# Kernel tuning notes

Hardware: AMD Instinct MI355X
Metric: run time of the kernel (lower is better)

Reference implementation:

```python
import jax, jax.numpy as jnp
import numpy as np

CH = 128
C2 = CH // 2
TEMP = 5.0
RATE = 2  # down conv: k=2,s=2,p=0 ; up: convtranspose k=2,s=2,p=0


def _down(x, w, b):
    # Conv2d(ch, ch, kernel=2, stride=2, pad=0) as a patch contraction
    B, C, H, W = x.shape
    xr = x.reshape(B, C, H // 2, 2, W // 2, 2)
    return jnp.einsum('bcipjq,ocpq->boij', xr, w) + b[None, :, None, None]


def _conv1x1(x, w):
    # w: [out, in]
    return jnp.einsum('bchw,oc->bohw', x, w)


def _maxpool2(x):
    B, C, H, W = x.shape
    return x.reshape(B, C, H // 2, 2, W // 2, 2).max(axis=(3, 5))


def _up(x, w, b):
    # ConvTranspose2d(ch, ch, kernel=2, stride=2, pad=0): each pixel -> 2x2 block
    # w: [in, out, 2, 2] (PyTorch layout)
    B, C, H, W = x.shape
    y = jnp.einsum('bchw,copq->bohpwq', x, w).reshape(B, w.shape[1], H * 2, W * 2)
    return y + b[None, :, None, None]


def setup_inputs() -> dict:
    key = jax.random.key(0)
    ks = jax.random.split(key, 12)
    B, H, W = 4, 192, 192
    sc = 0.05
    return {
        'input_x': jax.random.normal(ks[0], (B, CH, H, W), jnp.float32),
        'input_y': jax.random.normal(ks[1], (B, CH, H, W), jnp.float32),
        'down0_w': jax.random.normal(ks[2], (CH, CH, 2, 2), jnp.float32) * sc,
        'down0_b': jax.random.normal(ks[3], (CH,), jnp.float32) * sc,
        'down1_w': jax.random.normal(ks[4], (CH, CH, 2, 2), jnp.float32) * sc,
        'down1_b': jax.random.normal(ks[5], (CH,), jnp.float32) * sc,
        'theta_w': jax.random.normal(ks[6], (C2, CH), jnp.float32) * sc,
        'phi_w': jax.random.normal(ks[7], (C2, CH), jnp.float32) * sc,
        'g_w': jax.random.normal(ks[8], (C2, CH), jnp.float32) * sc,
        'o_w': jax.random.normal(ks[9], (CH, C2), jnp.float32) * sc,
        'up_w': jax.random.normal(ks[10], (CH, CH, 2, 2), jnp.float32) * sc,
        'up_b': jax.random.normal(ks[11], (CH,), jnp.float32) * sc,
        'gamma': jnp.float32(0.5),
    }


def reference(input_x, input_y, down0_w, down0_b, down1_w, down1_b,
              theta_w, phi_w, g_w, o_w, up_w, up_b, gamma):
    x = _down(input_x, down0_w, down0_b)          # [B, CH, h, w]
    y = _down(input_y, down1_w, down1_b)
    B, _, h, w = x.shape
    N = h * w
    M = N // 4

    theta = _conv1x1(x, theta_w).reshape(B, C2, N)          # queries
    phi = _maxpool2(_conv1x1(x, phi_w)).reshape(B, C2, M)   # keys (pooled)
    g = _maxpool2(_conv1x1(y, g_w)).reshape(B, C2, M)       # values (pooled)

    scores = jnp.einsum('bcn,bcm->bnm', theta, phi)          # [B, N, M]
    beta = jax.nn.softmax(TEMP * scores, axis=-1)

    o_map = jnp.einsum('bcm,bnm->bcn', g, beta).reshape(B, C2, h, w)
    o = _conv1x1(o_map, o_w)                                 # [B, CH, h, w]
    out = _up(o, up_w, up_b) + gamma * input_y
    return out
```

## Files before the change

kernel.cpp:

```cpp
#include <hip/hip_runtime.h>
#include <hip/hip_bf16.h>

#define NN    9216
#define MM    2304
#define HW    36864
#define SLABF 4718592
#define TEMPF 5.0f

#define OFF_X   0
#define OFF_Y   4718592
#define OFF_TH  9437184
#define OFF_TP  11796480
#define OFF_PH  14155776
#define OFF_G   14745600
#define OFF_OM  15335424

typedef unsigned short u16;
typedef unsigned int   u32;
typedef __attribute__((ext_vector_type(8))) short bf16x8;
typedef __attribute__((ext_vector_type(4))) float f32x4;

__device__ __forceinline__ u16 f2bf(float f){
  u32 u; __builtin_memcpy(&u,&f,4);
  u32 lsb = (u>>16)&1u; u += 0x7fffu + lsb;
  return (u16)(u>>16);
}
__device__ __forceinline__ u32 pkbf(float a, float b){
  union { __hip_bfloat162 h; u32 u; } v;
  v.h = __float22bfloat162_rn(make_float2(a,b));
  return v.u;
}

__global__ __launch_bounds__(256) void k_down(const float* __restrict__ in,
    const float* __restrict__ w, const float* __restrict__ bias, float* __restrict__ out)
{
  __shared__ __align__(16) float xs[2][6144];
  int blk = blockIdx.x;
  int jt = blk & 1;
  int r1 = blk >> 1;
  int i  = r1 % 96; int b = r1 / 96;
  int t  = threadIdx.x;

  const float* src = in + (size_t)b*128*HW + (size_t)(2*i)*192 + jt*96;

  int cl[3], qq[3];
  #pragma unroll
  for (int k = 0; k < 3; k++) {
    int idx = t + k*256;
    cl[k] = idx / 24;
    qq[k] = idx - cl[k]*24;
  }

  float4 va[3], vb[3];
  #pragma unroll
  for (int k = 0; k < 3; k++) {
    const float* p = src + (size_t)cl[k]*HW + qq[k]*4;
    va[k] = *(const float4*)p;
    vb[k] = *(const float4*)(p + 192);
  }
  #pragma unroll
  for (int k = 0; k < 3; k++) {
    float* d = &xs[0][cl[k]*192 + qq[k]*8];
    *(float4*)d       = make_float4(va[k].x, vb[k].x, va[k].y, vb[k].y);
    *(float4*)(d + 4) = make_float4(va[k].z, vb[k].z, va[k].w, vb[k].w);
  }

  int og = t >> 4, jg = t & 15;
  int o0 = og * 8;
  float acc[8][3];
  #pragma unroll
  for (int oo = 0; oo < 8; oo++)
    #pragma unroll
    for (int jj = 0; jj < 3; jj++) acc[oo][jj] = 0.f;

  const float* wbase = w + (size_t)o0*512;

  for (int ch = 0; ch < 4; ch++) {
    if (ch < 3) {
      #pragma unroll
      for (int k = 0; k < 3; k++) {
        const float* p = src + (size_t)((ch+1)*32 + cl[k])*HW + qq[k]*4;
        va[k] = *(const float4*)p;
        vb[k] = *(const float4*)(p + 192);
      }
    }
    __syncthreads();

    const float* xb = xs[ch & 1];
    const float* wc = wbase + (ch*32)*4;
    for (int c = 0; c < 32; c++) {
      const float* xp = xb + c*192 + jg*12;
      float4 xv0 = *(const float4*)(xp);
      float4 xv1 = *(const float4*)(xp + 4);
      float4 xv2 = *(const float4*)(xp + 8);
      const float* wp = wc + c*4;
      #pragma unroll
      for (int oo = 0; oo < 8; oo++) {
        float4 wv = *(const float4*)(wp + oo*512);
        acc[oo][0] += xv0.x*wv.x + xv0.z*wv.y + xv0.y*wv.z + xv0.w*wv.w;
        acc[oo][1] += xv1.x*wv.x + xv1.z*wv.y + xv1.y*wv.z + xv1.w*wv.w;
        acc[oo][2] += xv2.x*wv.x + xv2.z*wv.y + xv2.y*wv.z + xv2.w*wv.w;
      }
    }

    if (ch < 3) {
      #pragma unroll
      for (int k = 0; k < 3; k++) {
        float* d = &xs[(ch+1) & 1][cl[k]*192 + qq[k]*8];
        *(float4*)d       = make_float4(va[k].x, vb[k].x, va[k].y, vb[k].y);
        *(float4*)(d + 4) = make_float4(va[k].z, vb[k].z, va[k].w, vb[k].w);
      }
    }
  }

  #pragma unroll
  for (int oo = 0; oo < 8; oo++) {
    int o = o0 + oo;
    float bv = bias[o];
    float* op = out + ((size_t)(b*128 + o))*NN + i*96 + jt*48 + jg*3;
    op[0] = acc[oo][0] + bv;
    op[1] = acc[oo][1] + bv;
    op[2] = acc[oo][2] + bv;
  }
}

__global__ __launch_bounds__(256) void k_conv(const float* __restrict__ X,
    const float* __restrict__ WG, float* __restrict__ out)
{
  __shared__ __align__(16) float Xs[128*32];
  __shared__ __align__(16) float wt[128*64];
  int b  = blockIdx.x / 288;
  int n0 = (blockIdx.x % 288) * 32;
  int t  = threadIdx.x;
  for (int idx = t; idx < 8192; idx += 256) {
    int c = idx >> 6, cc = idx & 63;
    wt[idx] = WG[cc*128 + c];
  }
  for (int idx = t; idx < 1024; idx += 256) {
    int c = idx >> 3, wq = idx & 7;
    ((float4*)Xs)[idx] = *(const float4*)&X[((size_t)(b*128 + c))*NN + n0 + wq*4];
  }
  __syncthreads();
  int n = t & 31, og = t >> 5;
  float acc[8];
  #pragma unroll
  for (int k = 0; k < 8; k++) acc[k] = 0.f;
  for (int c = 0; c < 128; c++) {
    float xv = Xs[(c<<5) + n];
    const float* wrow = wt + (c<<6) + og*8;
    float4 wa = *(const float4*)wrow;
    float4 wb = *(const float4*)(wrow + 4);
    acc[0]+=wa.x*xv; acc[1]+=wa.y*xv; acc[2]+=wa.z*xv; acc[3]+=wa.w*xv;
    acc[4]+=wb.x*xv; acc[5]+=wb.y*xv; acc[6]+=wb.z*xv; acc[7]+=wb.w*xv;
  }
  #pragma unroll
  for (int k = 0; k < 8; k++)
    out[((size_t)(b*64 + og*8 + k))*NN + n0 + n] = acc[k];
}

__global__ __launch_bounds__(256) void k_pool(const float* __restrict__ in, float* __restrict__ out)
{
  int t = blockIdx.x*256 + threadIdx.x;
  int J = t % 48; int r = t/48; int I = r % 48; r /= 48; int cc = r & 63; int b = r >> 6;
  const float* p = in + ((size_t)(b*64+cc))*NN + (size_t)(2*I)*96 + 2*J;
  float m = fmaxf(fmaxf(p[0],p[1]), fmaxf(p[96],p[97]));
  out[((size_t)(b*64+cc))*MM + I*48 + J] = m;
}

__global__ __launch_bounds__(256) void k_attn(const float* __restrict__ TH,
    const float* __restrict__ PH, const float* __restrict__ G, float* __restrict__ OUT)
{
  __shared__ __align__(16) u16 sm[13824];
  int t = threadIdx.x;
  int lane = t & 63, wv = t >> 6;
  int quad = lane >> 4, l15 = lane & 15;
  int b  = blockIdx.x / 144;
  int q0 = (blockIdx.x % 144) * 64;
  int qw = q0 + wv*16;

  bf16x8 afrag[2];
  #pragma unroll
  for (int h = 0; h < 2; h++)
    #pragma unroll
    for (int j = 0; j < 8; j++) {
      float v = TEMPF * TH[((size_t)(b*64 + h*32 + quad*8 + j))*NN + qw + l15];
      afrag[h][j] = (short)f2bf(v);
    }

  f32x4 oacc[4];
  #pragma unroll
  for (int ct = 0; ct < 4; ct++)
    #pragma unroll
    for (int r = 0; r < 4; r++) oacc[ct][r] = 0.f;
  float m_r[4], l_r[4];
  #pragma unroll
  for (int r = 0; r < 4; r++) { m_r[r] = -3.0e38f; l_r[r] = 0.f; }

  int kth = t & 63;
  int cg  = t >> 6;

  for (int k0 = 0; k0 < MM; k0 += 64) {
    __syncthreads();
    #pragma unroll
    for (int h = 0; h < 2; h++) {
      int c0 = cg*16 + h*8;
      u32 pk[4];
      #pragma unroll
      for (int p = 0; p < 4; p++) {
        float f0 = PH[((size_t)(b*64 + c0 + 2*p    ))*MM + k0 + kth];
        float f1 = PH[((size_t)(b*64 + c0 + 2*p + 1))*MM + k0 + kth];
        pk[p] = pkbf(f0, f1);
      }
      *(uint4*)&sm[kth*72 + c0] = make_uint4(pk[0],pk[1],pk[2],pk[3]);
    }
    {
      int cc = t >> 2, kq = (t & 3) << 4;
      const float* gp = &G[((size_t)(b*64 + cc))*MM + k0 + kq];
      u32 w[8];
      #pragma unroll
      for (int p = 0; p < 8; p++) w[p] = pkbf(gp[2*p], gp[2*p+1]);
      *(uint4*)&sm[4608 + cc*72 + kq]     = make_uint4(w[0],w[1],w[2],w[3]);
      *(uint4*)&sm[4608 + cc*72 + kq + 8] = make_uint4(w[4],w[5],w[6],w[7]);
    }
    __syncthreads();

    f32x4 s[4];
    #pragma unroll
    for (int kt = 0; kt < 4; kt++) {
      f32x4 acc;
      #pragma unroll
      for (int r = 0; r < 4; r++) acc[r] = 0.f;
      #pragma unroll
      for (int h = 0; h < 2; h++) {
        bf16x8 bfrag = *(const bf16x8*)&sm[(kt*16 + l15)*72 + h*32 + quad*8];
        acc = __builtin_amdgcn_mfma_f32_16x16x32_bf16(afrag[h], bfrag, acc, 0, 0, 0);
      }
      s[kt] = acc;
    }

    float al[4];
    #pragma unroll
    for (int r = 0; r < 4; r++) {
      float mx = fmaxf(fmaxf(s[0][r], s[1][r]), fmaxf(s[2][r], s[3][r]));
      #pragma unroll
      for (int d = 1; d < 16; d <<= 1) mx = fmaxf(mx, __shfl_xor(mx, d));
      float mn = fmaxf(m_r[r], mx);
      float a  = __expf(m_r[r] - mn);
      m_r[r] = mn;
      float ps = 0.f;
      #pragma unroll
      for (int kt = 0; kt < 4; kt++) {
        float p = __expf(s[kt][r] - mn);
        s[kt][r] = p; ps += p;
      }
      #pragma unroll
      for (int d = 1; d < 16; d <<= 1) ps += __shfl_xor(ps, d);
      l_r[r] = l_r[r]*a + ps;
      al[r] = a;
    }
    #pragma unroll
    for (int kt = 0; kt < 4; kt++)
      #pragma unroll
      for (int r = 0; r < 4; r++)
        sm[9216 + wv*1152 + (quad*4 + r)*72 + kt*16 + l15] = f2bf(s[kt][r]);
    #pragma unroll
    for (int ct = 0; ct < 4; ct++)
      #pragma unroll
      for (int r = 0; r < 4; r++) oacc[ct][r] *= al[r];

    bf16x8 pf[2];
    #pragma unroll
    for (int h = 0; h < 2; h++)
      pf[h] = *(const bf16x8*)&sm[9216 + wv*1152 + l15*72 + h*32 + quad*8];
    #pragma unroll
    for (int ct = 0; ct < 4; ct++)
      #pragma unroll
      for (int h = 0; h < 2; h++) {
        bf16x8 gf = *(const bf16x8*)&sm[4608 + (ct*16 + l15)*72 + h*32 + quad*8];
        oacc[ct] = __builtin_amdgcn_mfma_f32_16x16x32_bf16(pf[h], gf, oacc[ct], 0, 0, 0);
      }
  }

  __syncthreads();
  float inv[4];
  #pragma unroll
  for (int r = 0; r < 4; r++) inv[r] = 1.0f / l_r[r];
  float* ol = (float*)sm + wv*1280;
  #pragma unroll
  for (int ct = 0; ct < 4; ct++)
    #pragma unroll
    for (int r = 0; r < 4; r++)
      ol[(ct*16 + l15)*20 + quad*4 + r] = oacc[ct][r] * inv[r];
  __syncthreads();
  const float* orow = ol + lane*20;
  float4 v0 = *(const float4*)(orow);
  float4 v1 = *(const float4*)(orow + 4);
  float4 v2 = *(const float4*)(orow + 8);
  float4 v3 = *(const float4*)(orow + 12);
  float* dst = &OUT[((size_t)(b*64 + lane))*NN + qw];
  *(float4*)(dst)      = v0;
  *(float4*)(dst + 4)  = v1;
  *(float4*)(dst + 8)  = v2;
  *(float4*)(dst + 12) = v3;
}

__global__ __launch_bounds__(256) void k_oconv(const float* __restrict__ X,
    const float* __restrict__ OW, float* __restrict__ dout)
{
  __shared__ __align__(16) float Xs[64*64];
  __shared__ __align__(16) float wt[64*128];
  int b  = blockIdx.x / 144;
  int n0 = (blockIdx.x % 144) * 64;
  int t  = threadIdx.x;
  for (int idx = t; idx < 8192; idx += 256) {
    int cc = idx >> 7, o = idx & 127;
    wt[idx] = OW[o*64 + cc];
  }
  for (int idx = t; idx < 1024; idx += 256) {
    int cc = idx >> 4, wq = idx & 15;
    ((float4*)Xs)[idx] = *(const float4*)&X[((size_t)(b*64 + cc))*NN + n0 + wq*4];
  }
  __syncthreads();
  int n = t & 63, og = t >> 6;
  float acc[32];
  #pragma unroll
  for (int k = 0; k < 32; k++) acc[k] = 0.f;
  for (int cc = 0; cc < 64; cc++) {
    float xv = Xs[(cc << 6) + n];
    const float* wrow = wt + (cc << 7) + og*32;
    #pragma unroll
    for (int k = 0; k < 32; k++) acc[k] += wrow[k]*xv;
  }
  int ng = n0 + n;
  int i = ng / 96, j = ng - (ng/96)*96;
  #pragma unroll
  for (int k = 0; k < 32; k++) {
    int o = og*32 + k;
    size_t addr = (size_t)b*SLABF + (size_t)(o>>2)*HW
                + (size_t)(2*i + ((o>>1)&1))*192 + 2*j + (o&1);
    dout[addr] = acc[k];
  }
}

__global__ __launch_bounds__(256) void k_up(float* __restrict__ dout,
    const float* __restrict__ upw, const float* __restrict__ upb,
    const float* __restrict__ Y, const float* __restrict__ gamma_p)
{
  __shared__ __align__(16) float o_s[128*96];
  int blk = blockIdx.x;
  int b = blk / 96, i = blk - b*96;
  int t = threadIdx.x;
  size_t slab = (size_t)b*SLABF;
  const float* src = dout + slab + (size_t)(2*i)*192;

  for (int idx = t; idx < 12288; idx += 256) {
    int run = idx / 384, rem = idx - run*384;
    int r = rem / 192, col = rem - r*192;
    float v = src[(size_t)run*HW + r*192 + col];
    int o = 4*run + 2*r + (col&1);
    o_s[o*96 + (col>>1)] = v;
  }
  __syncthreads();

  int op5 = t >> 3, jg = t & 7;
  float gm = *gamma_p;

  for (int opc = 0; opc < 4; opc++) {
    int op = opc*32 + op5;
    float bias = upb[op];
    size_t obase = slab + (size_t)op*HW + (size_t)(2*i)*192;
    for (int s = 0; s < 3; s++) {
      int j0 = jg*12 + s*4;
      float a00[4], a01[4], a10[4], a11[4];
      #pragma unroll
      for (int jj = 0; jj < 4; jj++) { a00[jj]=0.f; a01[jj]=0.f; a10[jj]=0.f; a11[jj]=0.f; }
      for (int c = 0; c < 128; c++) {
        float4 ov = *(const float4*)&o_s[c*96 + j0];
        float4 wv = *(const float4*)&upw[((size_t)c*128 + op)*4];
        a00[0]+=ov.x*wv.x; a01[0]+=ov.x*wv.y; a10[0]+=ov.x*wv.z; a11[0]+=ov.x*wv.w;
        a00[1]+=ov.y*wv.x; a01[1]+=ov.y*wv.y; a10[1]+=ov.y*wv.z; a11[1]+=ov.y*wv.w;
        a00[2]+=ov.z*wv.x; a01[2]+=ov.z*wv.y; a10[2]+=ov.z*wv.z; a11[2]+=ov.z*wv.w;
        a00[3]+=ov.w*wv.x; a01[3]+=ov.w*wv.y; a10[3]+=ov.w*wv.z; a11[3]+=ov.w*wv.w;
      }
      size_t p0 = obase + 2*j0;
      size_t p1 = p0 + 192;
      float4 y0a = *(const float4*)&Y[p0];
      float4 y0b = *(const float4*)&Y[p0 + 4];
      float4 y1a = *(const float4*)&Y[p1];
      float4 y1b = *(const float4*)&Y[p1 + 4];
      *(float4*)&dout[p0]     = make_float4(a00[0]+bias+gm*y0a.x, a01[0]+bias+gm*y0a.y,
                                            a00[1]+bias+gm*y0a.z, a01[1]+bias+gm*y0a.w);
      *(float4*)&dout[p0 + 4] = make_float4(a00[2]+bias+gm*y0b.x, a01[2]+bias+gm*y0b.y,
                                            a00[3]+bias+gm*y0b.z, a01[3]+bias+gm*y0b.w);
      *(float4*)&dout[p1]     = make_float4(a10[0]+bias+gm*y1a.x, a11[0]+bias+gm*y1a.y,
                                            a10[1]+bias+gm*y1a.z, a11[1]+bias+gm*y1a.w);
      *(float4*)&dout[p1 + 4] = make_float4(a10[2]+bias+gm*y1b.x, a11[2]+bias+gm*y1b.y,
                                            a10[3]+bias+gm*y1b.z, a11[3]+bias+gm*y1b.w);
    }
  }
}

extern "C" void kernel_launch(void* const* d_in, const int* in_sizes, int n_in,
                              void* d_out, int out_size, void* d_ws, size_t ws_size,
                              hipStream_t stream) {
  const float* x_in  = (const float*)d_in[0];
  const float* y_in  = (const float*)d_in[1];
  const float* d0w   = (const float*)d_in[2];
  const float* d0b   = (const float*)d_in[3];
  const float* d1w   = (const float*)d_in[4];
  const float* d1b   = (const float*)d_in[5];
  const float* thw   = (const float*)d_in[6];
  const float* phw   = (const float*)d_in[7];
  const float* gw    = (const float*)d_in[8];
  const float* ow    = (const float*)d_in[9];
  const float* upw   = (const float*)d_in[10];
  const float* upb   = (const float*)d_in[11];
  const float* gamma = (const float*)d_in[12];
  float* out = (float*)d_out;

  k_down <<<768,  256, 0, stream>>>(x_in, d0w, d0b, out + OFF_X);
  k_down <<<768,  256, 0, stream>>>(y_in, d1w, d1b, out + OFF_Y);
  k_conv <<<1152, 256, 0, stream>>>(out + OFF_X, thw, out + OFF_TH);
  k_conv <<<1152, 256, 0, stream>>>(out + OFF_X, phw, out + OFF_TP);
  k_pool <<<2304, 256, 0, stream>>>(out + OFF_TP, out + OFF_PH);
  k_conv <<<1152, 256, 0, stream>>>(out + OFF_Y, gw, out + OFF_TP);
  k_pool <<<2304, 256, 0, stream>>>(out + OFF_TP, out + OFF_G);
  k_attn <<<576,  256, 0, stream>>>(out + OFF_TH, out + OFF_PH, out + OFF_G, out + OFF_OM);
  k_oconv<<<576,  256, 0, stream>>>(out + OFF_OM, ow, out);
  k_up   <<<384,  256, 0, stream>>>(out, upw, upb, y_in, gamma);
}
```

Baseline: 786.9 us.

## Split up-conv rows into half-width blocks and remap threads for coalesced weights

The transposed-conv kernel now processes half a row per block, doubling the grid to 768 blocks and halving shared memory. Threads are remapped so the 32 lanes covering consecutive output channels read contiguous weight float4s. Each thread computes 6 input columns for one output channel in a single pass over channels, instead of three passes of 4 columns. The aim is more parallelism across CUs and fewer redundant weight loads. The cost is more accumulator registers per thread and strided float2 reads from shared memory.

```diff
diff --git a/kernel.cpp b/kernel.cpp
--- a/kernel.cpp
+++ b/kernel.cpp
@@ -346,56 +346,63 @@
     const float* __restrict__ upw, const float* __restrict__ upb,
     const float* __restrict__ Y, const float* __restrict__ gamma_p)
 {
-  __shared__ __align__(16) float o_s[128*96];
+  __shared__ __align__(16) float o_s[128*48];
   int blk = blockIdx.x;
-  int b = blk / 96, i = blk - b*96;
+  int jh = blk & 1;
+  int r1 = blk >> 1;
+  int i = r1 % 96, b = r1 / 96;
   int t = threadIdx.x;
   size_t slab = (size_t)b*SLABF;
-  const float* src = dout + slab + (size_t)(2*i)*192;
-
-  for (int idx = t; idx < 12288; idx += 256) {
-    int run = idx / 384, rem = idx - run*384;
-    int r = rem / 192, col = rem - r*192;
-    float v = src[(size_t)run*HW + r*192 + col];
-    int o = 4*run + 2*r + (col&1);
-    o_s[o*96 + (col>>1)] = v;
+  const float* src = dout + slab + (size_t)(2*i)*192 + jh*96;
+
+  for (int idx = t; idx < 6144; idx += 256) {
+    int run = idx / 192, rem = idx - run*192;
+    int r = rem / 96, cl = rem - r*96;
+    float v = src[(size_t)run*HW + r*192 + cl];
+    int o = 4*run + 2*r + (cl&1);
+    o_s[o*48 + (cl>>1)] = v;
   }
   __syncthreads();
 
-  int op5 = t >> 3, jg = t & 7;
+  int op_l = t & 31, jg = t >> 5;
   float gm = *gamma_p;
 
-  for (int opc = 0; opc < 4; opc++) {
-    int op = opc*32 + op5;
+  for (int oc = 0; oc < 4; oc++) {
+    int op = oc*32 + op_l;
+    float a0[12], a1[12];
+    #pragma unroll
+    for (int k = 0; k < 12; k++) { a0[k] = 0.f; a1[k] = 0.f; }
+
+    const float* wp = upw + (size_t)op*4;
+    const float* xb = o_s + jg*6;
+    for (int c = 0; c < 128; c++) {
+      float4 wv = *(const float4*)(wp + (size_t)c*512);
+      const float* xp = xb + c*48;
+      float2 x01 = *(const float2*)(xp);
+      float2 x23 = *(const float2*)(xp + 2);
+      float2 x45 = *(const float2*)(xp + 4);
+      a0[0] += x01.x*wv.x; a0[1] += x01.x*wv.y; a1[0] += x01.x*wv.z; a1[1] += x01.x*wv.w;
+      a0[2] += x01.y*wv.x; a0[3] += x01.y*wv.y; a1[2] += x01.y*wv.z; a1[3] += x01.y*wv.w;
+      a0[4] += x23.x*wv.x; a0[5] += x23.x*wv.y; a1[4] += x23.x*wv.z; a1[5] += x23.x*wv.w;
+      a0[6] += x23.y*wv.x; a0[7] += x23.y*wv.y; a1[6] += x23.y*wv.z; a1[7] += x23.y*wv.w;
+      a0[8] += x45.x*wv.x; a0[9] += x45.x*wv.y; a1[8] += x45.x*wv.z; a1[9] += x45.x*wv.w;
+      a0[10]+= x45.y*wv.x; a0[11]+= x45.y*wv.y; a1[10]+= x45.y*wv.z; a1[11]+= x45.y*wv.w;
+    }
+
     float bias = upb[op];
-    size_t obase = slab + (size_t)op*HW + (size_t)(2*i)*192;
-    for (int s = 0; s < 3; s++) {
-      int j0 = jg*12 + s*4;
-      float a00[4], a01[4], a10[4], a11[4];
-      #pragma unroll
-      for (int jj = 0; jj < 4; jj++) { a00[jj]=0.f; a01[jj]=0.f; a10[jj]=0.f; a11[jj]=0.f; }
-      for (int c = 0; c < 128; c++) {
-        float4 ov = *(const float4*)&o_s[c*96 + j0];
-        float4 wv = *(const float4*)&upw[((size_t)c*128 + op)*4];
-        a00[0]+=ov.x*wv.x; a01[0]+=ov.x*wv.y; a10[0]+=ov.x*wv.z; a11[0]+=ov.x*wv.w;
-        a00[1]+=ov.y*wv.x; a01[1]+=ov.y*wv.y; a10[1]+=ov.y*wv.z; a11[1]+=ov.y*wv.w;
-        a00[2]+=ov.z*wv.x; a01[2]+=ov.z*wv.y; a10[2]+=ov.z*wv.z; a11[2]+=ov.z*wv.w;
-        a00[3]+=ov.w*wv.x; a01[3]+=ov.w*wv.y; a10[3]+=ov.w*wv.z; a11[3]+=ov.w*wv.w;
-      }
-      size_t p0 = obase + 2*j0;
-      size_t p1 = p0 + 192;
-      float4 y0a = *(const float4*)&Y[p0];
-      float4 y0b = *(const float4*)&Y[p0 + 4];
-      float4 y1a = *(const float4*)&Y[p1];
-      float4 y1b = *(const float4*)&Y[p1 + 4];
-      *(float4*)&dout[p0]     = make_float4(a00[0]+bias+gm*y0a.x, a01[0]+bias+gm*y0a.y,
-                                            a00[1]+bias+gm*y0a.z, a01[1]+bias+gm*y0a.w);
-      *(float4*)&dout[p0 + 4] = make_float4(a00[2]+bias+gm*y0b.x, a01[2]+bias+gm*y0b.y,
-                                            a00[3]+bias+gm*y0b.z, a01[3]+bias+gm*y0b.w);
-      *(float4*)&dout[p1]     = make_float4(a10[0]+bias+gm*y1a.x, a11[0]+bias+gm*y1a.y,
-                                            a10[1]+bias+gm*y1a.z, a11[1]+bias+gm*y1a.w);
-      *(float4*)&dout[p1 + 4] = make_float4(a10[2]+bias+gm*y1b.x, a11[2]+bias+gm*y1b.y,
-                                            a10[3]+bias+gm*y1b.z, a11[3]+bias+gm*y1b.w);
+    size_t obase = slab + (size_t)op*HW + (size_t)(2*i)*192 + jh*96 + jg*12;
+    float* p0 = dout + obase;
+    float* p1 = p0 + 192;
+    const float* y0 = Y + obase;
+    const float* y1 = y0 + 192;
+    #pragma unroll
+    for (int q = 0; q < 3; q++) {
+      float4 ya = *(const float4*)(y0 + 4*q);
+      float4 yb = *(const float4*)(y1 + 4*q);
+      *(float4*)(p0 + 4*q) = make_float4(a0[4*q+0]+bias+gm*ya.x, a0[4*q+1]+bias+gm*ya.y,
+                                         a0[4*q+2]+bias+gm*ya.z, a0[4*q+3]+bias+gm*ya.w);
+      *(float4*)(p1 + 4*q) = make_float4(a1[4*q+0]+bias+gm*yb.x, a1[4*q+1]+bias+gm*yb.y,
+                                         a1[4*q+2]+bias+gm*yb.z, a1[4*q+3]+bias+gm*yb.w);
     }
   }
 }
@@ -427,5 +434,5 @@
   k_pool <<<2304, 256, 0, stream>>>(out + OFF_TP, out + OFF_G);
   k_attn <<<576,  256, 0, stream>>>(out + OFF_TH, out + OFF_PH, out + OFF_G, out + OFF_OM);
   k_oconv<<<576,  256, 0, stream>>>(out + OFF_OM, ow, out);
-  k_up   <<<384,  256, 0, stream>>>(out, upw, upb, y_in, gamma);
-}
+  k_up   <<<768,  256, 0, stream>>>(out, upw, upb, y_in, gamma);
+}
```

Result: faster. 720.1 us (-8.5%).
